# Performance work log

Hardware: AMD Instinct MI355X
Metric: run time of the kernel (lower is better)

The kernel has to match this reference:

```python
import jax, jax.numpy as jnp
import numpy as np

# ---- static config (matches init_kwargs) ----
B, N, DIM = 1, 2048, 1024
H, KVH, D = 16, 8, 64
GQ = H // KVH                 # grouped queries per kv head
WS = 64                       # sliding window size (causal, exact)
CBS, STRIDE = 32, 16          # compress block size / sliding stride
SEL_BLK, NSEL, NMEM = 32, 4, 1
NCB = N // STRIDE             # num compressed blocks (128)
NFB = N // SEL_BLK            # num fine blocks (64)
NCPF = SEL_BLK // STRIDE      # compressed blocks per fine block (2)
HID = CBS * D                 # compress MLP hidden (expand factor 1.0)
SCALE = D ** -0.5
THETA = 10000.0
NEG = -jnp.finfo(jnp.float32).max


def setup_inputs():
    key = jax.random.key(0)
    ks = jax.random.split(key, 16)
    s = 0.02
    r = lambda i, shape: jax.random.normal(ks[i], shape, jnp.float32) * s
    return {
        "inp": jax.random.normal(ks[0], (B, N, DIM), jnp.float32),
        "norm_g": jnp.ones((DIM,), jnp.float32),
        "Wqkv": r(1, (DIM, (H + 2 * KVH) * D)),
        "mem_kv": r(2, (2, KVH, NMEM, D)),
        "k_pos": r(3, (KVH, CBS, D)),
        "v_pos": r(4, (KVH, CBS, D)),
        "kW1": r(5, (CBS * D, HID)), "kb1": jnp.zeros((HID,), jnp.float32),
        "kW2": r(6, (HID, D)), "kb2": jnp.zeros((D,), jnp.float32),
        "vW1": r(7, (CBS * D, HID)), "vb1": jnp.zeros((HID,), jnp.float32),
        "vW2": r(8, (HID, D)), "vb2": jnp.zeros((D,), jnp.float32),
        "combW": r(9, (DIM, 3 * H)),
        "combB": jnp.tile(jnp.array([-2.0, -2.0, 2.0], jnp.float32), H),
        "Wout": r(10, (H * D, DIM)),
    }


def _rope(t):
    # lucidrains rotary-embedding-torch: interleaved adjacent-pair rotation
    inv_freq = 1.0 / (THETA ** (jnp.arange(0, D, 2, dtype=jnp.float32) / D))
    ang = jnp.arange(N, dtype=jnp.float32)[:, None] * inv_freq        # [N, D/2]
    cos = jnp.repeat(jnp.cos(ang), 2, axis=-1)                        # [N, D]
    sin = jnp.repeat(jnp.sin(ang), 2, axis=-1)
    t2 = t.reshape(*t.shape[:-1], D // 2, 2)
    rot = jnp.stack([-t2[..., 1], t2[..., 0]], axis=-1).reshape(t.shape)
    return t * cos + rot * sin


def _forward(inp, norm_g, Wqkv, mem_kv, k_pos, v_pos,
             kW1, kb1, kW2, kb2, vW1, vb1, vW2, vb2,
             combW, combB, Wout):
    # RMSNorm
    x = inp * jax.lax.rsqrt(jnp.mean(inp * inp, -1, keepdims=True)
                            + jnp.finfo(inp.dtype).eps) * norm_g
    qkv = x @ Wqkv
    q, k, v = jnp.split(qkv, [H * D, H * D + KVH * D], axis=-1)
    q = q.reshape(B, N, H, D).transpose(0, 2, 1, 3)      # b h n d
    k = k.reshape(B, N, KVH, D).transpose(0, 2, 1, 3)    # b kvh n d
    v = v.reshape(B, N, KVH, D).transpose(0, 2, 1, 3)

    # ---- compressed branch (overlapping windows, left zero pad) ----
    overlap = CBS - STRIDE
    kp = jnp.pad(k, ((0, 0), (0, 0), (overlap, 0), (0, 0)))
    vp = jnp.pad(v, ((0, 0), (0, 0), (overlap, 0), (0, 0)))
    widx = jnp.arange(NCB)[:, None] * STRIDE + jnp.arange(CBS)[None, :]  # [NCB, CBS]
    kw = kp[:, :, widx] + k_pos[None, :, None]   # b kvh w cbs d
    vw = vp[:, :, widx] + v_pos[None, :, None]

    def cmlp(t, W1, b1, W2, b2):
        t = t.reshape(B, KVH, NCB, CBS * D)
        return jax.nn.relu(t @ W1 + b1) @ W2 + b2       # b kvh w d

    ck = cmlp(kw, kW1, kb1, kW2, kb2)
    cv = cmlp(vw, vW1, vb1, vW2, vb2)
    ck = jnp.concatenate([jnp.broadcast_to(mem_kv[0], (B, KVH, NMEM, D)), ck], 2)
    cv = jnp.concatenate([jnp.broadcast_to(mem_kv[1], (B, KVH, NMEM, D)), cv], 2)

    qg = q.reshape(B, KVH, GQ, N, D)
    csim = jnp.einsum('bhgid,bhjd->bhgij', qg, ck) * SCALE   # no mask (cmask=None)
    cattn = jax.nn.softmax(csim, -1)
    cout = jnp.einsum('bhgij,bhjd->bhgid', cattn, cv).reshape(B, H, N, D)

    # rotary AFTER compressed attention (as in source)
    rq, rk = _rope(q), _rope(k)

    # ---- importance scores -> top-k fine block selection ----
    imp = csim[..., NMEM:].mean(2)                          # b kvh n NCB (share grouped q)
    imp = imp.reshape(B, KVH, N, NFB, NCPF).mean(-1)        # mean-pool to fine blocks
    q_blk = jnp.arange(N) // SEL_BLK
    diag = q_blk[:, None] == jnp.arange(NFB)[None, :]
    imp = jnp.where(diag[None, None], NEG, imp)             # mask own (diagonal) block
    imp = jax.nn.softmax(jnp.pad(imp, ((0, 0),) * 3 + ((1, 0),),
                                 constant_values=-1000.0), -1)[..., 1:]
    sel_val, sel_idx = jax.lax.top_k(imp, NSEL)             # b kvh n NSEL

    # ---- fine (block-selected) attention ----
    own = jnp.broadcast_to(q_blk[None, None, :, None], (B, KVH, N, 1))
    sel_idx = jnp.concatenate([sel_idx, own], -1)           # append own block
    fmask = jnp.repeat((sel_val > 1e-10)[..., None], SEL_BLK, -1)  # b kvh n NSEL blk
    causal_row = jnp.tril(jnp.ones((SEL_BLK, SEL_BLK), bool))[jnp.arange(N) % SEL_BLK]
    causal = jnp.broadcast_to(causal_row[None, None, :, None, :],
                              (B, KVH, N, 1, SEL_BLK))
    fmask = jnp.concatenate([fmask, causal], 3).reshape(B, KVH, N, (NSEL + 1) * SEL_BLK)

    fk_blocks = rk.reshape(B, KVH, NFB, SEL_BLK, D)
    fv_blocks = v.reshape(B, KVH, NFB, SEL_BLK, D)
    gather = jax.vmap(jax.vmap(lambda blocks, idx: blocks[idx]))  # over b, kvh
    fk = gather(fk_blocks, sel_idx).reshape(B, KVH, N, (NSEL + 1) * SEL_BLK, D)
    fv = gather(fv_blocks, sel_idx).reshape(B, KVH, N, (NSEL + 1) * SEL_BLK, D)

    rqg = rq.reshape(B, KVH, GQ, N, D)
    fsim = jnp.einsum('bhgid,bhijd->bhgij', rqg, fk) * SCALE
    fsim = jnp.where(fmask[:, :, None], fsim, NEG / 10)
    fattn = jax.nn.softmax(fsim, -1)
    fout = jnp.einsum('bhgij,bhijd->bhgid', fattn, fv).reshape(B, H, N, D)

    # ---- sliding window (causal, exact window size WS) ----
    NW = N // WS
    kp2 = jnp.pad(rk, ((0, 0), (0, 0), (WS, 0), (0, 0)))
    vp2 = jnp.pad(v, ((0, 0), (0, 0), (WS, 0), (0, 0)))
    kidx = jnp.arange(NW)[:, None] * WS + jnp.arange(2 * WS)[None, :]
    kwin = kp2[:, :, kidx]                                  # b kvh nw 2ws d
    vwin = vp2[:, :, kidx]
    qwin = rqg.reshape(B, KVH, GQ, NW, WS, D)
    ssim = jnp.einsum('bhgwid,bhwjd->bhgwij', qwin, kwin) * SCALE
    i = jnp.arange(WS)[:, None]
    j = jnp.arange(2 * WS)[None, :]
    diff = i - (j - WS)
    local_ok = (diff >= 0) & (diff < WS)                    # [WS, 2WS]
    keypos = jnp.arange(NW)[:, None, None] * WS + (jnp.arange(2 * WS) - WS)[None, None, :]
    smask = local_ok[None] & (keypos >= 0)                  # [NW, WS, 2WS]
    ssim = jnp.where(smask[None, None, None], ssim, NEG)
    sattn = jax.nn.softmax(ssim, -1)
    sout = jnp.einsum('bhgwij,bhwjd->bhgwid', sattn, vwin).reshape(B, H, N, D)

    # ---- learned strategy combination (compressed, fine, sliding) ----
    gates = jax.nn.sigmoid(x @ combW + combB).reshape(B, N, H, 3).transpose(0, 2, 1, 3)
    out = gates[..., 0:1] * cout + gates[..., 1:2] * fout + gates[..., 2:3] * sout
    out = out.transpose(0, 2, 1, 3).reshape(B, N, H * D) @ Wout
    return out


def reference(inp, norm_g, Wqkv, mem_kv, k_pos, v_pos,
              kW1, kb1, kW2, kb2, vW1, vb1, vW2, vb2,
              combW, combB, Wout):
    return _forward(inp, norm_g, Wqkv, mem_kv, k_pos, v_pos,
                    kW1, kb1, kW2, kb2, vW1, vb1, vW2, vb2,
                    combW, combB, Wout)
```

## Files before the change

### kernel.cpp

```cpp
#include <hip/hip_runtime.h>
#include <hip/hip_bf16.h>

#define NTOK 2048
#define DIM 1024
#define NH 16
#define KVH 8
#define GQ 2
#define HD 64
#define WS 64
#define CBS 32
#define STRIDE 16
#define SEL_BLK 32
#define NSEL 4
#define NMEM 1
#define NCB 128
#define NFB 64
#define HIDN 2048
#define SCALE 0.125f
#define NEGF (-3.4028234663852886e38f)
#define NEG10F (-3.4028234663852886e37f)

typedef __attribute__((ext_vector_type(8))) short bf16x8;
typedef __attribute__((ext_vector_type(4))) float f32x4;

__device__ __forceinline__ float bflo(unsigned u) { return __uint_as_float(u << 16); }
__device__ __forceinline__ float bfhi(unsigned u) { return __uint_as_float(u & 0xffff0000u); }
__device__ __forceinline__ void dot8(const float4& qa, const float4& qb, uint4 a, float& s) {
    s += qa.x * bflo(a.x) + qa.y * bfhi(a.x) + qa.z * bflo(a.y) + qa.w * bfhi(a.y) +
         qb.x * bflo(a.z) + qb.y * bfhi(a.z) + qb.z * bflo(a.w) + qb.w * bfhi(a.w);
}

__global__ __launch_bounds__(256) void rmsnorm_kernel(const float* __restrict__ inp,
                                                      const float* __restrict__ g,
                                                      float* __restrict__ x,
                                                      __hip_bfloat16* __restrict__ xb) {
    int n = blockIdx.x;
    const float* row = inp + (size_t)n * DIM;
    float ss = 0.f;
    for (int c = threadIdx.x; c < DIM; c += 256) { float v = row[c]; ss += v * v; }
    __shared__ float red[4];
    for (int o = 32; o; o >>= 1) ss += __shfl_down(ss, o, 64);
    if ((threadIdx.x & 63) == 0) red[threadIdx.x >> 6] = ss;
    __syncthreads();
    if (threadIdx.x == 0) red[0] = red[0] + red[1] + red[2] + red[3];
    __syncthreads();
    float rs = 1.0f / sqrtf(red[0] / (float)DIM + 1.1920928955078125e-07f);
    float* xr = x + (size_t)n * DIM;
    __hip_bfloat16* xbr = xb + (size_t)n * DIM;
    for (int c = threadIdx.x; c < DIM; c += 256) {
        float v = row[c] * rs * g[c];
        xr[c] = v;
        xbr[c] = __float2bfloat16(v);
    }
}

__device__ __forceinline__ void transpose_body(const float* __restrict__ B,
                                               __hip_bfloat16* __restrict__ Bt,
                                               int K, int N, int bx, int by) {
    __shared__ float tile[32][33];
    int n0 = bx * 32, k0 = by * 32;
    int x = threadIdx.x & 31, y = threadIdx.x >> 5;
    for (int i = 0; i < 4; i++) {
        int k = k0 + y + 8 * i, n = n0 + x;
        tile[y + 8 * i][x] = (k < K && n < N) ? B[(size_t)k * N + n] : 0.f;
    }
    __syncthreads();
    for (int i = 0; i < 4; i++) {
        int n = n0 + y + 8 * i, k = k0 + x;
        if (n < N && k < K) Bt[(size_t)n * K + k] = __float2bfloat16(tile[x][y + 8 * i]);
    }
}

__global__ __launch_bounds__(256) void transpose_all_kernel(
    const float* Wqkv, __hip_bfloat16* Wqkvt,
    const float* kW1, __hip_bfloat16* kW1t,
    const float* vW1, __hip_bfloat16* vW1t,
    const float* Wout, __hip_bfloat16* Woutt,
    const float* combW, __hip_bfloat16* combWt,
    const float* kW2, __hip_bfloat16* kW2t,
    const float* vW2, __hip_bfloat16* vW2t) {
    int b = blockIdx.x;
    if (b < 2048) { transpose_body(Wqkv, Wqkvt, 1024, 2048, b % 64, b / 64); return; }
    b -= 2048;
    if (b < 4096) { transpose_body(kW1, kW1t, 2048, 2048, b % 64, b / 64); return; }
    b -= 4096;
    if (b < 4096) { transpose_body(vW1, vW1t, 2048, 2048, b % 64, b / 64); return; }
    b -= 4096;
    if (b < 1024) { transpose_body(Wout, Woutt, 1024, 1024, b % 32, b / 32); return; }
    b -= 1024;
    if (b < 64) { transpose_body(combW, combWt, 1024, 48, b % 2, b / 2); return; }
    b -= 64;
    if (b < 128) { transpose_body(kW2, kW2t, 2048, 64, b % 2, b / 2); return; }
    b -= 128;
    transpose_body(vW2, vW2t, 2048, 64, b % 2, b / 2);
}

template <int ACT, int OUTBF16>
__device__ __forceinline__ void mfma_gemm_body(const __hip_bfloat16* __restrict__ A,
                                               const __hip_bfloat16* __restrict__ Bt,
                                               const float* __restrict__ bias,
                                               void* __restrict__ Cp,
                                               int M, int N, int K, int bx, int by) {
    __shared__ __align__(16) short As[128 * 32];
    __shared__ __align__(16) short Bs[128 * 32];
    int tid = threadIdx.x;
    int lane = tid & 63, wave = tid >> 6;
    int wm = (wave >> 1) * 64, wn = (wave & 1) * 64;
    int m0 = by * 128, n0 = bx * 128;
    f32x4 acc[4][4];
    for (int r = 0; r < 4; r++)
        for (int c = 0; c < 4; c++)
            acc[r][c] = (f32x4){0.f, 0.f, 0.f, 0.f};

    int r0 = tid >> 2, kc0 = tid & 3;
    int r1 = (tid + 256) >> 2, kc1 = tid & 3;

    for (int k0 = 0; k0 < K; k0 += 32) {
        __syncthreads();
        *(uint4*)&As[r0 * 32 + kc0 * 8] =
            *(const uint4*)(A + (size_t)(m0 + r0) * K + k0 + kc0 * 8);
        *(uint4*)&As[r1 * 32 + kc1 * 8] =
            *(const uint4*)(A + (size_t)(m0 + r1) * K + k0 + kc1 * 8);
        *(uint4*)&Bs[r0 * 32 + kc0 * 8] =
            *(const uint4*)(Bt + (size_t)(n0 + r0) * K + k0 + kc0 * 8);
        *(uint4*)&Bs[r1 * 32 + kc1 * 8] =
            *(const uint4*)(Bt + (size_t)(n0 + r1) * K + k0 + kc1 * 8);
        __syncthreads();
        bf16x8 af[4], bfr[4];
#pragma unroll
        for (int r = 0; r < 4; r++)
            af[r] = *(const bf16x8*)&As[(wm + r * 16 + (lane & 15)) * 32 + (lane >> 4) * 8];
#pragma unroll
        for (int c = 0; c < 4; c++)
            bfr[c] = *(const bf16x8*)&Bs[(wn + c * 16 + (lane & 15)) * 32 + (lane >> 4) * 8];
#pragma unroll
        for (int r = 0; r < 4; r++)
#pragma unroll
            for (int c = 0; c < 4; c++)
                acc[r][c] = __builtin_amdgcn_mfma_f32_16x16x32_bf16(af[r], bfr[c], acc[r][c], 0, 0, 0);
    }
    for (int r = 0; r < 4; r++) {
        int grow = m0 + wm + r * 16 + (lane >> 4) * 4;
        for (int c = 0; c < 4; c++) {
            int gcol = n0 + wn + c * 16 + (lane & 15);
            float bv = bias ? bias[gcol] : 0.f;
#pragma unroll
            for (int v = 0; v < 4; v++) {
                float val = acc[r][c][v] + bv;
                if (ACT == 1) val = fmaxf(val, 0.f);
                if (OUTBF16)
                    ((__hip_bfloat16*)Cp)[(size_t)(grow + v) * N + gcol] = __float2bfloat16(val);
                else
                    ((float*)Cp)[(size_t)(grow + v) * N + gcol] = val;
            }
        }
    }
}

template <int ACT, int OUTBF16>
__global__ __launch_bounds__(256) void mfma_gemm(const __hip_bfloat16* __restrict__ A,
                                                 const __hip_bfloat16* __restrict__ Bt,
                                                 const float* __restrict__ bias,
                                                 void* __restrict__ Cp,
                                                 int M, int N, int K) {
    mfma_gemm_body<ACT, OUTBF16>(A, Bt, bias, Cp, M, N, K, blockIdx.x, blockIdx.y);
}

__global__ __launch_bounds__(256) void mfma_gemm_pair(const __hip_bfloat16* A0,
                                                      const __hip_bfloat16* A1,
                                                      const __hip_bfloat16* Bt0,
                                                      const __hip_bfloat16* Bt1,
                                                      const float* bias0, const float* bias1,
                                                      __hip_bfloat16* C0, __hip_bfloat16* C1,
                                                      int M, int N, int K) {
    if (blockIdx.z == 0)
        mfma_gemm_body<1, 1>(A0, Bt0, bias0, C0, M, N, K, blockIdx.x, blockIdx.y);
    else
        mfma_gemm_body<1, 1>(A1, Bt1, bias1, C1, M, N, K, blockIdx.x, blockIdx.y);
}

__device__ __forceinline__ void skgemm_body(const __hip_bfloat16* __restrict__ A,
                                            const __hip_bfloat16* __restrict__ Bt,
                                            float* __restrict__ C,
                                            int M, int Nout, int K, int by, int bz, int nz) {
    __shared__ __align__(16) short As[128 * 32];
    __shared__ __align__(16) short Bs[64 * 32];
    int tid = threadIdx.x;
    int lane = tid & 63, wave = tid >> 6;
    int m0 = by * 128;
    int wm = wave * 32;
    int kchunk = K / nz;
    int kbase = bz * kchunk;
    f32x4 acc[2][4];
    for (int r = 0; r < 2; r++)
        for (int c = 0; c < 4; c++) acc[r][c] = (f32x4){0.f, 0.f, 0.f, 0.f};

    int ra = tid >> 2, kc = (tid & 3) * 8;
    for (int k0 = kbase; k0 < kbase + kchunk; k0 += 32) {
        __syncthreads();
        *(uint4*)&As[ra * 32 + kc] = *(const uint4*)(A + (size_t)(m0 + ra) * K + k0 + kc);
        *(uint4*)&As[(ra + 64) * 32 + kc] =
            *(const uint4*)(A + (size_t)(m0 + ra + 64) * K + k0 + kc);
        uint4 bv = (uint4){0u, 0u, 0u, 0u};
        if (ra < Nout) bv = *(const uint4*)(Bt + (size_t)ra * K + k0 + kc);
        *(uint4*)&Bs[ra * 32 + kc] = bv;
        __syncthreads();
        bf16x8 af[2], bfr[4];
#pragma unroll
        for (int r = 0; r < 2; r++)
            af[r] = *(const bf16x8*)&As[(wm + r * 16 + (lane & 15)) * 32 + (lane >> 4) * 8];
#pragma unroll
        for (int c = 0; c < 4; c++)
            bfr[c] = *(const bf16x8*)&Bs[(c * 16 + (lane & 15)) * 32 + (lane >> 4) * 8];
#pragma unroll
        for (int r = 0; r < 2; r++)
#pragma unroll
            for (int c = 0; c < 4; c++)
                acc[r][c] = __builtin_amdgcn_mfma_f32_16x16x32_bf16(af[r], bfr[c], acc[r][c], 0, 0, 0);
    }
    for (int r = 0; r < 2; r++) {
        int grow = m0 + wm + r * 16 + (lane >> 4) * 4;
        for (int c = 0; c < 4; c++) {
            int gcol = c * 16 + (lane & 15);
            if (gcol >= Nout) continue;
#pragma unroll
            for (int v = 0; v < 4; v++)
                atomicAdd(&C[(size_t)(grow + v) * Nout + gcol], acc[r][c][v]);
        }
    }
}

__global__ __launch_bounds__(256) void skgemm_kernel(const __hip_bfloat16* __restrict__ A,
                                                     const __hip_bfloat16* __restrict__ Bt,
                                                     float* __restrict__ C,
                                                     int M, int Nout, int K) {
    skgemm_body(A, Bt, C, M, Nout, K, blockIdx.y, blockIdx.z, gridDim.z);
}

__global__ __launch_bounds__(256) void skgemm_pair(const __hip_bfloat16* A0,
                                                   const __hip_bfloat16* A1,
                                                   const __hip_bfloat16* Bt0,
                                                   const __hip_bfloat16* Bt1,
                                                   float* C0, float* C1,
                                                   int M, int Nout, int K) {
    if (blockIdx.x == 0)
        skgemm_body(A0, Bt0, C0, M, Nout, K, blockIdx.y, blockIdx.z, gridDim.z);
    else
        skgemm_body(A1, Bt1, C1, M, Nout, K, blockIdx.y, blockIdx.z, gridDim.z);
}

__global__ __launch_bounds__(256) void initbias2_kernel(float* __restrict__ C0,
                                                        const float* __restrict__ b0,
                                                        float* __restrict__ C1,
                                                        const float* __restrict__ b1,
                                                        int M, int Nout) {
    int idx = blockIdx.x * 256 + threadIdx.x;
    int tot = M * Nout;
    if (idx < tot) C0[idx] = b0[idx % Nout];
    else if (idx < 2 * tot) { idx -= tot; C1[idx] = b1[idx % Nout]; }
}

__global__ __launch_bounds__(256) void initbias_kernel(float* __restrict__ C,
                                                       const float* __restrict__ bias,
                                                       int M, int Nout) {
    int idx = blockIdx.x * 256 + threadIdx.x;
    if (idx < M * Nout) C[idx] = bias[idx % Nout];
}

__global__ __launch_bounds__(256) void buildwin_kernel(const float* __restrict__ qkv,
                                                       const float* __restrict__ k_pos,
                                                       const float* __restrict__ v_pos,
                                                       __hip_bfloat16* __restrict__ kwflat,
                                                       __hip_bfloat16* __restrict__ vwflat) {
    size_t total = (size_t)(KVH * NCB) * HIDN;
    for (size_t e = (size_t)blockIdx.x * 256 + threadIdx.x; e < total;
         e += (size_t)gridDim.x * 256) {
        int r = (int)(e >> 11);
        int c = (int)(e & 2047);
        int j = c >> 6, d = c & 63;
        int h = r >> 7, i = r & 127;
        int p = i * STRIDE + j - (CBS - STRIDE);
        float kb = k_pos[((size_t)h * CBS + j) * HD + d];
        float vb = v_pos[((size_t)h * CBS + j) * HD + d];
        float kv = 0.f, vv = 0.f;
        if (p >= 0) {
            kv = qkv[(size_t)p * 2048 + 1024 + h * HD + d];
            vv = qkv[(size_t)p * 2048 + 1536 + h * HD + d];
        }
        kwflat[e] = __float2bfloat16(kv + kb);
        vwflat[e] = __float2bfloat16(vv + vb);
    }
}

__global__ __launch_bounds__(256) void rope_kernel(const float* __restrict__ qkv,
                                                   float* __restrict__ rq,
                                                   __hip_bfloat16* __restrict__ rk,
                                                   __hip_bfloat16* __restrict__ vt) {
    int n = blockIdx.x;
    int t = threadIdx.x;
    for (int idx = t; idx < NH * 32; idx += 256) {
        int h = idx >> 5, f = idx & 31;
        float inv = exp2f((float)f * -0.41524101186092f);
        float ang = (float)n * inv;
        float cc = cosf(ang), ssn = sinf(ang);
        float a = qkv[(size_t)n * 2048 + h * HD + 2 * f];
        float b = qkv[(size_t)n * 2048 + h * HD + 2 * f + 1];
        float* o = rq + ((size_t)h * NTOK + n) * HD + 2 * f;
        o[0] = a * cc - b * ssn;
        o[1] = b * cc + a * ssn;
    }
    for (int idx = t; idx < KVH * 32; idx += 256) {
        int h = idx >> 5, f = idx & 31;
        float inv = exp2f((float)f * -0.41524101186092f);
        float ang = (float)n * inv;
        float cc = cosf(ang), ssn = sinf(ang);
        float a = qkv[(size_t)n * 2048 + 1024 + h * HD + 2 * f];
        float b = qkv[(size_t)n * 2048 + 1024 + h * HD + 2 * f + 1];
        __hip_bfloat16* o = rk + ((size_t)h * NTOK + n) * HD + 2 * f;
        o[0] = __float2bfloat16(a * cc - b * ssn);
        o[1] = __float2bfloat16(b * cc + a * ssn);
    }
    for (int idx = t; idx < KVH * HD; idx += 256) {
        int h = idx >> 6, d = idx & 63;
        vt[((size_t)h * NTOK + n) * HD + d] =
            __float2bfloat16(qkv[(size_t)n * 2048 + 1536 + h * HD + d]);
    }
}

__global__ __launch_bounds__(256) void cattn2_kernel(const float* __restrict__ qkv,
                                                     const float* __restrict__ ckraw,
                                                     const float* __restrict__ cvraw,
                                                     const float* __restrict__ memkv,
                                                     float* __restrict__ cout,
                                                     float* __restrict__ imp) {
    int h = blockIdx.x >> 6;
    int i0 = (blockIdx.x & 63) * 32;
    int t = threadIdx.x;
    __shared__ float qs[64][68];
    __shared__ float sc[64][132];
    __shared__ float scratch[32 * 68];
    __shared__ float memk[64], memv[64];
    __shared__ float impm[32], impd[32];

    for (int idx = t; idx < 4096; idx += 256) {
        int row = idx >> 6, d = idx & 63;
        int g = row >> 5, qi = row & 31;
        qs[row][d] = qkv[(size_t)(i0 + qi) * 2048 + (h * 2 + g) * 64 + d];
    }
    if (t < 64) { memk[t] = memkv[h * 64 + t]; memv[t] = memkv[(8 + h) * 64 + t]; }
    __syncthreads();
    if (t < 64) {
        float s = 0.f;
        for (int d = 0; d < 64; d++) s += qs[t][d] * memk[d];
        sc[t][0] = s * SCALE;
    }
    int rg = t >> 3, kg = t & 7;
    for (int c = 0; c < 4; c++) {
        __syncthreads();
        for (int idx = t; idx < 2048; idx += 256) {
            int jj = idx >> 6, d = idx & 63;
            scratch[jj * 68 + d] = ckraw[((size_t)h * 128 + c * 32 + jj) * 64 + d];
        }
        __syncthreads();
        float a0[4] = {}, a1[4] = {};
        for (int d = 0; d < 64; d += 4) {
            float4 q0 = *(const float4*)&qs[rg * 2][d];
            float4 q1 = *(const float4*)&qs[rg * 2 + 1][d];
#pragma unroll
            for (int kk = 0; kk < 4; kk++) {
                float4 kv = *(const float4*)&scratch[(kg + kk * 8) * 68 + d];
                a0[kk] += q0.x * kv.x + q0.y * kv.y + q0.z * kv.z + q0.w * kv.w;
                a1[kk] += q1.x * kv.x + q1.y * kv.y + q1.z * kv.z + q1.w * kv.w;
            }
        }
#pragma unroll
        for (int kk = 0; kk < 4; kk++) {
            sc[rg * 2][1 + c * 32 + kg + kk * 8] = a0[kk] * SCALE;
            sc[rg * 2 + 1][1 + c * 32 + kg + kk * 8] = a1[kk] * SCALE;
        }
    }
    __syncthreads();
    for (int idx = t; idx < 2048; idx += 256) {
        int qi = idx >> 6, fb = idx & 63;
        float v = 0.25f * (sc[qi][1 + 2 * fb] + sc[qi][2 + 2 * fb] +
                           sc[32 + qi][1 + 2 * fb] + sc[32 + qi][2 + 2 * fb]);
        if (fb == ((i0 + qi) >> 5)) v = NEGF;
        scratch[qi * 66 + fb] = v;
    }
    __syncthreads();
    if (t < 32) {
        float m = -1000.f;
        for (int j = 0; j < 64; j++) m = fmaxf(m, scratch[t * 66 + j]);
        float den = expf(-1000.f - m);
        for (int j = 0; j < 64; j++) den += expf(scratch[t * 66 + j] - m);
        impm[t] = m; impd[t] = 1.f / den;
    } else if (t >= 64 && t < 128) {
        int r = t - 64;
        float m = NEGF;
        for (int j = 0; j < 129; j++) m = fmaxf(m, sc[r][j]);
        float den = 0.f;
        for (int j = 0; j < 129; j++) { float e = expf(sc[r][j] - m); sc[r][j] = e; den += e; }
        float inv = 1.f / den;
        for (int j = 0; j < 129; j++) sc[r][j] *= inv;
    }
    __syncthreads();
    for (int idx = t; idx < 2048; idx += 256) {
        int qi = idx >> 6, fb = idx & 63;
        imp[((size_t)h * NTOK + i0 + qi) * 64 + fb] =
            expf(scratch[qi * 66 + fb] - impm[qi]) * impd[qi];
    }
    int dg = t & 7;
    float o0[8], o1[8];
    {
        float p0 = sc[rg * 2][0], p1 = sc[rg * 2 + 1][0];
#pragma unroll
        for (int dd = 0; dd < 8; dd++) {
            float v = memv[dg + dd * 8];
            o0[dd] = p0 * v;
            o1[dd] = p1 * v;
        }
    }
    for (int c = 0; c < 4; c++) {
        __syncthreads();
        for (int idx = t; idx < 2048; idx += 256) {
            int jj = idx >> 6, d = idx & 63;
            scratch[jj * 68 + d] = cvraw[((size_t)h * 128 + c * 32 + jj) * 64 + d];
        }
        __syncthreads();
        for (int jj = 0; jj < 32; jj++) {
            float p0 = sc[rg * 2][1 + c * 32 + jj];
            float p1 = sc[rg * 2 + 1][1 + c * 32 + jj];
#pragma unroll
            for (int dd = 0; dd < 8; dd++) {
                float v = scratch[jj * 68 + dg + dd * 8];
                o0[dd] += p0 * v;
                o1[dd] += p1 * v;
            }
        }
    }
    {
        int row = rg * 2;
        int g = row >> 5, qi = row & 31;
        int g2 = (row + 1) >> 5, qi2 = (row + 1) & 31;
#pragma unroll
        for (int dd = 0; dd < 8; dd++) {
            cout[(((size_t)(h * 2 + g)) * NTOK + i0 + qi) * 64 + dd * 8 + dg] = o0[dd];
            cout[(((size_t)(h * 2 + g2)) * NTOK + i0 + qi2) * 64 + dd * 8 + dg] = o1[dd];
        }
    }
}

__global__ __launch_bounds__(256) void topk_kernel(const float* __restrict__ imp,
                                                   int* __restrict__ selidx,
                                                   int* __restrict__ selmask) {
    int idx = blockIdx.x * 256 + threadIdx.x;
    if (idx >= KVH * NTOK) return;
    const float* ip = imp + (size_t)idx * NFB;
    float v[NFB];
    for (int j = 0; j < NFB; j++) v[j] = ip[j];
    unsigned long long taken = 0ull;
    int mk = 0;
    int i = idx & 2047;
    for (int p = 0; p < NSEL; p++) {
        float bv = NEGF;
        int bi = 0;
        for (int j = 0; j < NFB; j++) {
            if (!((taken >> j) & 1ull) && v[j] > bv) { bv = v[j]; bi = j; }
        }
        taken |= 1ull << bi;
        selidx[(size_t)idx * 5 + p] = bi;
        if (bv > 1e-10f) mk |= 1 << p;
    }
    selidx[(size_t)idx * 5 + 4] = i >> 5;
    selmask[idx] = mk;
}

__global__ __launch_bounds__(256) void attn_fused_kernel(const float* __restrict__ rq,
                                                         const __hip_bfloat16* __restrict__ rk,
                                                         const __hip_bfloat16* __restrict__ vt,
                                                         const int* __restrict__ selidx,
                                                         const int* __restrict__ selmask,
                                                         float* __restrict__ fout,
                                                         float* __restrict__ sout) {
    int ws = threadIdx.x >> 6, lane = threadIdx.x & 63;
    __shared__ float sp[4][2][160];
    __shared__ int sel[4][5];
    __shared__ int smk[4];
    float* p0 = sp[ws][0];
    float* p1 = sp[ws][1];

    int kq = lane >> 2, c = lane & 3;
    int kv8 = lane >> 3, c8 = lane & 7;

    if (blockIdx.x < 4096) {
        int wid = blockIdx.x * 4 + ws;
        int h = wid >> 11, i = wid & 2047;
        if (lane < 5) sel[ws][lane] = selidx[((size_t)h * NTOK + i) * 5 + lane];
        if (lane == 5) smk[ws] = selmask[h * NTOK + i];

        const float* q0p = rq + ((size_t)(h * 2 + 0) * NTOK + i) * 64 + c * 16;
        const float* q1p = rq + ((size_t)(h * 2 + 1) * NTOK + i) * 64 + c * 16;
        float4 q0[4], q1[4];
#pragma unroll
        for (int u = 0; u < 4; u++) {
            q0[u] = *(const float4*)(q0p + u * 4);
            q1[u] = *(const float4*)(q1p + u * 4);
        }
        __syncthreads();
        int mk = smk[ws];
        int iq = i & 31;
#pragma unroll
        for (int kt = 0; kt < 10; kt++) {
            int slot = kt >> 1;
            int blk = sel[ws][slot];
            int key = kt * 16 + kq;
            int jj = key & 31;
            int kpos = blk * 32 + jj;
            bool valid = (slot < 4) ? (((mk >> slot) & 1) != 0) : (jj <= iq);
            const __hip_bfloat16* kr = rk + ((size_t)h * NTOK + kpos) * 64 + c * 16;
            float s0 = 0.f, s1 = 0.f;
            uint4 a = *(const uint4*)(kr);
            uint4 b = *(const uint4*)(kr + 8);
            dot8(q0[0], q0[1], a, s0); dot8(q0[2], q0[3], b, s0);
            dot8(q1[0], q1[1], a, s1); dot8(q1[2], q1[3], b, s1);
            s0 += __shfl_xor(s0, 1); s0 += __shfl_xor(s0, 2);
            s1 += __shfl_xor(s1, 1); s1 += __shfl_xor(s1, 2);
            if (c == 0) {
                p0[key] = valid ? s0 * SCALE : NEG10F;
                p1[key] = valid ? s1 * SCALE : NEG10F;
            }
        }
        __syncthreads();
        {
            float a0 = p0[lane], b0 = p0[lane + 64];
            float c0 = (lane < 32) ? p0[lane + 128] : NEG10F;
            float a1 = p1[lane], b1 = p1[lane + 64];
            float c1 = (lane < 32) ? p1[lane + 128] : NEG10F;
            float m0 = fmaxf(fmaxf(a0, b0), c0);
            float m1 = fmaxf(fmaxf(a1, b1), c1);
#pragma unroll
            for (int o = 1; o < 64; o <<= 1) {
                m0 = fmaxf(m0, __shfl_xor(m0, o));
                m1 = fmaxf(m1, __shfl_xor(m1, o));
            }
            float ea0 = __expf(a0 - m0), eb0 = __expf(b0 - m0), ec0 = (lane < 32) ? __expf(c0 - m0) : 0.f;
            float ea1 = __expf(a1 - m1), eb1 = __expf(b1 - m1), ec1 = (lane < 32) ? __expf(c1 - m1) : 0.f;
            float d0 = ea0 + eb0 + ec0;
            float d1 = ea1 + eb1 + ec1;
#pragma unroll
            for (int o = 1; o < 64; o <<= 1) {
                d0 += __shfl_xor(d0, o);
                d1 += __shfl_xor(d1, o);
            }
            float inv0 = 1.f / d0, inv1 = 1.f / d1;
            p0[lane] = ea0 * inv0; p0[lane + 64] = eb0 * inv0;
            p1[lane] = ea1 * inv1; p1[lane + 64] = eb1 * inv1;
            if (lane < 32) { p0[lane + 128] = ec0 * inv0; p1[lane + 128] = ec1 * inv1; }
        }
        __syncthreads();
        float o0[8] = {}, o1[8] = {};
#pragma unroll
        for (int slot = 0; slot < 5; slot++) {
            const __hip_bfloat16* vbase = vt + ((size_t)h * NTOK + sel[ws][slot] * 32) * 64;
#pragma unroll
            for (int pass = 0; pass < 4; pass++) {
                int j = pass * 8 + kv8;
                uint4 v = *(const uint4*)(vbase + j * 64 + c8 * 8);
                float pa = p0[slot * 32 + j], pb = p1[slot * 32 + j];
                float e0 = bflo(v.x), e1 = bfhi(v.x), e2 = bflo(v.y), e3 = bfhi(v.y);
                float e4 = bflo(v.z), e5 = bfhi(v.z), e6 = bflo(v.w), e7 = bfhi(v.w);
                o0[0] = fmaf(pa, e0, o0[0]); o0[1] = fmaf(pa, e1, o0[1]);
                o0[2] = fmaf(pa, e2, o0[2]); o0[3] = fmaf(pa, e3, o0[3]);
                o0[4] = fmaf(pa, e4, o0[4]); o0[5] = fmaf(pa, e5, o0[5]);
                o0[6] = fmaf(pa, e6, o0[6]); o0[7] = fmaf(pa, e7, o0[7]);
                o1[0] = fmaf(pb, e0, o1[0]); o1[1] = fmaf(pb, e1, o1[1]);
                o1[2] = fmaf(pb, e2, o1[2]); o1[3] = fmaf(pb, e3, o1[3]);
                o1[4] = fmaf(pb, e4, o1[4]); o1[5] = fmaf(pb, e5, o1[5]);
                o1[6] = fmaf(pb, e6, o1[6]); o1[7] = fmaf(pb, e7, o1[7]);
            }
        }
#pragma unroll
        for (int o = 8; o <= 32; o <<= 1)
#pragma unroll
            for (int d = 0; d < 8; d++) {
                o0[d] += __shfl_xor(o0[d], o);
                o1[d] += __shfl_xor(o1[d], o);
            }
        if (kv8 == 0) {
            float* f0 = fout + ((size_t)(h * 2 + 0) * NTOK + i) * 64 + c8 * 8;
            float* f1 = fout + ((size_t)(h * 2 + 1) * NTOK + i) * 64 + c8 * 8;
            *(float4*)(f0) = (float4){o0[0], o0[1], o0[2], o0[3]};
            *(float4*)(f0 + 4) = (float4){o0[4], o0[5], o0[6], o0[7]};
            *(float4*)(f1) = (float4){o1[0], o1[1], o1[2], o1[3]};
            *(float4*)(f1 + 4) = (float4){o1[4], o1[5], o1[6], o1[7]};
        }
    } else {
        int wid = (blockIdx.x - 4096) * 4 + ws;
        int h = wid >> 11, i = wid & 2047;
        const float* q0p = rq + ((size_t)(h * 2 + 0) * NTOK + i) * 64 + c * 16;
        const float* q1p = rq + ((size_t)(h * 2 + 1) * NTOK + i) * 64 + c * 16;
        float4 q0[4], q1[4];
#pragma unroll
        for (int u = 0; u < 4; u++) {
            q0[u] = *(const float4*)(q0p + u * 4);
            q1[u] = *(const float4*)(q1p + u * 4);
        }
#pragma unroll
        for (int kt = 0; kt < 4; kt++) {
            int key = kt * 16 + kq;
            int kpos = i - 63 + key;
            int kp = kpos < 0 ? 0 : kpos;
            const __hip_bfloat16* kr = rk + ((size_t)h * NTOK + kp) * 64 + c * 16;
            float s0 = 0.f, s1 = 0.f;
            uint4 a = *(const uint4*)(kr);
            uint4 b = *(const uint4*)(kr + 8);
            dot8(q0[0], q0[1], a, s0); dot8(q0[2], q0[3], b, s0);
            dot8(q1[0], q1[1], a, s1); dot8(q1[2], q1[3], b, s1);
            s0 += __shfl_xor(s0, 1); s0 += __shfl_xor(s0, 2);
            s1 += __shfl_xor(s1, 1); s1 += __shfl_xor(s1, 2);
            if (c == 0) {
                p0[key] = (kpos >= 0) ? s0 * SCALE : NEG10F;
                p1[key] = (kpos >= 0) ? s1 * SCALE : NEG10F;
            }
        }
        __syncthreads();
        {
            float a0 = p0[lane], a1 = p1[lane];
            float m0 = a0, m1 = a1;
#pragma unroll
            for (int o = 1; o < 64; o <<= 1) {
                m0 = fmaxf(m0, __shfl_xor(m0, o));
                m1 = fmaxf(m1, __shfl_xor(m1, o));
            }
            float e0 = __expf(a0 - m0), e1 = __expf(a1 - m1);
            float d0 = e0, d1 = e1;
#pragma unroll
            for (int o = 1; o < 64; o <<= 1) {
                d0 += __shfl_xor(d0, o);
                d1 += __shfl_xor(d1, o);
            }
            p0[lane] = e0 / d0;
            p1[lane] = e1 / d1;
        }
        __syncthreads();
        int base = i - 63;
        float o0[8] = {}, o1[8] = {};
        const __hip_bfloat16* vbase = vt + (size_t)h * NTOK * 64;
#pragma unroll
        for (int pass = 0; pass < 8; pass++) {
            int j = pass * 8 + kv8;
            int kpos = base + j;
            int kp = kpos < 0 ? 0 : kpos;
            uint4 v = *(const uint4*)(vbase + (size_t)kp * 64 + c8 * 8);
            float pa = p0[j], pb = p1[j];
            float e0 = bflo(v.x), e1 = bfhi(v.x), e2 = bflo(v.y), e3 = bfhi(v.y);
            float e4 = bflo(v.z), e5 = bfhi(v.z), e6 = bflo(v.w), e7 = bfhi(v.w);
            o0[0] = fmaf(pa, e0, o0[0]); o0[1] = fmaf(pa, e1, o0[1]);
            o0[2] = fmaf(pa, e2, o0[2]); o0[3] = fmaf(pa, e3, o0[3]);
            o0[4] = fmaf(pa, e4, o0[4]); o0[5] = fmaf(pa, e5, o0[5]);
            o0[6] = fmaf(pa, e6, o0[6]); o0[7] = fmaf(pa, e7, o0[7]);
            o1[0] = fmaf(pb, e0, o1[0]); o1[1] = fmaf(pb, e1, o1[1]);
            o1[2] = fmaf(pb, e2, o1[2]); o1[3] = fmaf(pb, e3, o1[3]);
            o1[4] = fmaf(pb, e4, o1[4]); o1[5] = fmaf(pb, e5, o1[5]);
            o1[6] = fmaf(pb, e6, o1[6]); o1[7] = fmaf(pb, e7, o1[7]);
        }
#pragma unroll
        for (int o = 8; o <= 32; o <<= 1)
#pragma unroll
            for (int d = 0; d < 8; d++) {
                o0[d] += __shfl_xor(o0[d], o);
                o1[d] += __shfl_xor(o1[d], o);
            }
        if (kv8 == 0) {
            float* s0p = sout + ((size_t)(h * 2 + 0) * NTOK + i) * 64 + c8 * 8;
            float* s1p = sout + ((size_t)(h * 2 + 1) * NTOK + i) * 64 + c8 * 8;
            *(float4*)(s0p) = (float4){o0[0], o0[1], o0[2], o0[3]};
            *(float4*)(s0p + 4) = (float4){o0[4], o0[5], o0[6], o0[7]};
            *(float4*)(s1p) = (float4){o1[0], o1[1], o1[2], o1[3]};
            *(float4*)(s1p + 4) = (float4){o1[4], o1[5], o1[6], o1[7]};
        }
    }
}

__global__ __launch_bounds__(256) void combine_kernel(const float* __restrict__ gateslin,
                                                      const float* __restrict__ cout,
                                                      const float* __restrict__ fout,
                                                      const float* __restrict__ sout,
                                                      __hip_bfloat16* __restrict__ att) {
    int n = blockIdx.x;
    for (int c = threadIdx.x; c < NH * HD; c += 256) {
        int hd = c >> 6, d = c & 63;
        float g0 = 1.f / (1.f + expf(-gateslin[(size_t)n * (NH * 3) + hd * 3 + 0]));
        float g1 = 1.f / (1.f + expf(-gateslin[(size_t)n * (NH * 3) + hd * 3 + 1]));
        float g2 = 1.f / (1.f + expf(-gateslin[(size_t)n * (NH * 3) + hd * 3 + 2]));
        size_t o = ((size_t)hd * NTOK + n) * HD + d;
        att[(size_t)n * (NH * HD) + c] =
            __float2bfloat16(g0 * cout[o] + g1 * fout[o] + g2 * sout[o]);
    }
}

extern "C" void kernel_launch(void* const* d_in, const int* in_sizes, int n_in,
                              void* d_out, int out_size, void* d_ws, size_t ws_size,
                              hipStream_t stream) {
    const float* inp    = (const float*)d_in[0];
    const float* norm_g = (const float*)d_in[1];
    const float* Wqkv   = (const float*)d_in[2];
    const float* mem_kv = (const float*)d_in[3];
    const float* k_pos  = (const float*)d_in[4];
    const float* v_pos  = (const float*)d_in[5];
    const float* kW1    = (const float*)d_in[6];
    const float* kb1    = (const float*)d_in[7];
    const float* kW2    = (const float*)d_in[8];
    const float* kb2    = (const float*)d_in[9];
    const float* vW1    = (const float*)d_in[10];
    const float* vb1    = (const float*)d_in[11];
    const float* vW2    = (const float*)d_in[12];
    const float* vb2    = (const float*)d_in[13];
    const float* combW  = (const float*)d_in[14];
    const float* combB  = (const float*)d_in[15];
    const float* Wout   = (const float*)d_in[16];
    float* out = (float*)d_out;

    char* base = (char*)d_ws;
    size_t off = 0;
    auto alloc = [&](size_t bytes) {
        void* p = base + off;
        off += (bytes + 255) & ~(size_t)255;
        return p;
    };
    float* x            = (float*)alloc((size_t)NTOK * DIM * 4);
    __hip_bfloat16* xb  = (__hip_bfloat16*)alloc((size_t)NTOK * DIM * 2);
    float* qkv          = (float*)alloc((size_t)NTOK * 2048 * 4);
    __hip_bfloat16* Wqkvt = (__hip_bfloat16*)alloc((size_t)2048 * 1024 * 2);
    __hip_bfloat16* kW1t  = (__hip_bfloat16*)alloc((size_t)2048 * 2048 * 2);
    __hip_bfloat16* vW1t  = (__hip_bfloat16*)alloc((size_t)2048 * 2048 * 2);
    __hip_bfloat16* Woutt = (__hip_bfloat16*)alloc((size_t)1024 * 1024 * 2);
    __hip_bfloat16* combWt = (__hip_bfloat16*)alloc((size_t)48 * 1024 * 2);
    __hip_bfloat16* kW2t  = (__hip_bfloat16*)alloc((size_t)64 * 2048 * 2);
    __hip_bfloat16* vW2t  = (__hip_bfloat16*)alloc((size_t)64 * 2048 * 2);
    __hip_bfloat16* kwflat = (__hip_bfloat16*)alloc((size_t)KVH * NCB * HIDN * 2);
    __hip_bfloat16* vwflat = (__hip_bfloat16*)alloc((size_t)KVH * NCB * HIDN * 2);
    __hip_bfloat16* hidkb = (__hip_bfloat16*)alloc((size_t)KVH * NCB * HIDN * 2);
    __hip_bfloat16* hidvb = (__hip_bfloat16*)alloc((size_t)KVH * NCB * HIDN * 2);
    float* ckraw        = (float*)alloc((size_t)KVH * NCB * HD * 4);
    float* cvraw        = (float*)alloc((size_t)KVH * NCB * HD * 4);
    float* rq           = (float*)alloc((size_t)NH * NTOK * HD * 4);
    __hip_bfloat16* rk  = (__hip_bfloat16*)alloc((size_t)KVH * NTOK * HD * 2);
    __hip_bfloat16* vt  = (__hip_bfloat16*)alloc((size_t)KVH * NTOK * HD * 2);
    float* coutb        = (float*)alloc((size_t)NH * NTOK * HD * 4);
    float* foutb        = (float*)alloc((size_t)NH * NTOK * HD * 4);
    float* soutb        = (float*)alloc((size_t)NH * NTOK * HD * 4);
    float* impb         = (float*)alloc((size_t)KVH * NTOK * NFB * 4);
    float* gatesb       = (float*)alloc((size_t)NTOK * NH * 3 * 4);
    __hip_bfloat16* attb = (__hip_bfloat16*)alloc((size_t)NTOK * DIM * 2);
    int* selidx         = (int*)alloc((size_t)KVH * NTOK * 5 * 4);
    int* selmask        = (int*)alloc((size_t)KVH * NTOK * 4);
    (void)ws_size; (void)in_sizes; (void)n_in; (void)out_size;

    rmsnorm_kernel<<<NTOK, 256, 0, stream>>>(inp, norm_g, x, xb);
    transpose_all_kernel<<<11584, 256, 0, stream>>>(Wqkv, Wqkvt, kW1, kW1t, vW1, vW1t,
                                                    Wout, Woutt, combW, combWt,
                                                    kW2, kW2t, vW2, vW2t);
    mfma_gemm<0, 0><<<dim3(16, 16), 256, 0, stream>>>(xb, Wqkvt, nullptr, qkv, 2048, 2048, 1024);
    initbias_kernel<<<(NTOK * 48 + 255) / 256, 256, 0, stream>>>(gatesb, combB, NTOK, 48);
    skgemm_kernel<<<dim3(1, 16, 4), 256, 0, stream>>>(xb, combWt, gatesb, 2048, 48, 1024);
    buildwin_kernel<<<4096, 256, 0, stream>>>(qkv, k_pos, v_pos, kwflat, vwflat);
    mfma_gemm_pair<<<dim3(16, 8, 2), 256, 0, stream>>>(kwflat, vwflat, kW1t, vW1t,
                                                       kb1, vb1, hidkb, hidvb,
                                                       1024, 2048, 2048);
    initbias2_kernel<<<(2 * 1024 * 64 + 255) / 256, 256, 0, stream>>>(ckraw, kb2, cvraw, vb2, 1024, 64);
    skgemm_pair<<<dim3(2, 8, 8), 256, 0, stream>>>(hidkb, hidvb, kW2t, vW2t,
                                                   ckraw, cvraw, 1024, 64, 2048);
    rope_kernel<<<NTOK, 256, 0, stream>>>(qkv, rq, rk, vt);
    cattn2_kernel<<<KVH * (NTOK / 32), 256, 0, stream>>>(qkv, ckraw, cvraw, mem_kv, coutb, impb);
    topk_kernel<<<(KVH * NTOK) / 256, 256, 0, stream>>>(impb, selidx, selmask);
    attn_fused_kernel<<<8192, 256, 0, stream>>>(rq, rk, vt, selidx, selmask, foutb, soutb);
    combine_kernel<<<NTOK, 256, 0, stream>>>(gatesb, coutb, foutb, soutb, attb);
    mfma_gemm<0, 0><<<dim3(8, 16), 256, 0, stream>>>(attb, Woutt, nullptr, out, 2048, 1024, 1024);
}
```

Before: 423.8 us.

## Fuse top-k selection into compressed attention and use direct global-to-LDS loads

Top-k block selection moves into the compressed-attention kernel and runs on the raw scores, so the importance matrix is never written to global memory and one kernel launch goes away. Selection compares raw scores, which gives the same order as softmax probabilities, and the mask threshold is recomputed from the softmax. The GEMM kernels now stage tiles with global_load_lds instead of loading into registers and then storing to LDS. Fast __expf replaces expf. The top-k loop runs serially on 32 threads per block, which adds latency to that kernel.

```diff
diff --git a/kernel.cpp b/kernel.cpp
--- a/kernel.cpp
+++ b/kernel.cpp
@@ -28,6 +28,11 @@
 __device__ __forceinline__ void dot8(const float4& qa, const float4& qb, uint4 a, float& s) {
     s += qa.x * bflo(a.x) + qa.y * bfhi(a.x) + qa.z * bflo(a.y) + qa.w * bfhi(a.y) +
          qb.x * bflo(a.z) + qb.y * bfhi(a.z) + qb.z * bflo(a.w) + qb.w * bfhi(a.w);
+}
+
+__device__ __forceinline__ void gload_lds16(const void* g, void* l) {
+    __builtin_amdgcn_global_load_lds((const __attribute__((address_space(1))) unsigned*)g,
+                                     (__attribute__((address_space(3))) unsigned*)l, 16, 0, 0);
 }
 
 __global__ __launch_bounds__(256) void rmsnorm_kernel(const float* __restrict__ inp,
@@ -112,19 +117,15 @@
         for (int c = 0; c < 4; c++)
             acc[r][c] = (f32x4){0.f, 0.f, 0.f, 0.f};
 
-    int r0 = tid >> 2, kc0 = tid & 3;
-    int r1 = (tid + 256) >> 2, kc1 = tid & 3;
+    int r0 = tid >> 2, kc0 = (tid & 3) * 8;
+    int r1 = r0 + 64;
 
     for (int k0 = 0; k0 < K; k0 += 32) {
         __syncthreads();
-        *(uint4*)&As[r0 * 32 + kc0 * 8] =
-            *(const uint4*)(A + (size_t)(m0 + r0) * K + k0 + kc0 * 8);
-        *(uint4*)&As[r1 * 32 + kc1 * 8] =
-            *(const uint4*)(A + (size_t)(m0 + r1) * K + k0 + kc1 * 8);
-        *(uint4*)&Bs[r0 * 32 + kc0 * 8] =
-            *(const uint4*)(Bt + (size_t)(n0 + r0) * K + k0 + kc0 * 8);
-        *(uint4*)&Bs[r1 * 32 + kc1 * 8] =
-            *(const uint4*)(Bt + (size_t)(n0 + r1) * K + k0 + kc1 * 8);
+        gload_lds16(A + (size_t)(m0 + r0) * K + k0 + kc0, &As[r0 * 32 + kc0]);
+        gload_lds16(A + (size_t)(m0 + r1) * K + k0 + kc0, &As[r1 * 32 + kc0]);
+        gload_lds16(Bt + (size_t)(n0 + r0) * K + k0 + kc0, &Bs[r0 * 32 + kc0]);
+        gload_lds16(Bt + (size_t)(n0 + r1) * K + k0 + kc0, &Bs[r1 * 32 + kc0]);
         __syncthreads();
         bf16x8 af[4], bfr[4];
 #pragma unroll
@@ -196,14 +197,12 @@
         for (int c = 0; c < 4; c++) acc[r][c] = (f32x4){0.f, 0.f, 0.f, 0.f};
 
     int ra = tid >> 2, kc = (tid & 3) * 8;
+    int rb = ra < Nout ? ra : Nout - 1;
     for (int k0 = kbase; k0 < kbase + kchunk; k0 += 32) {
         __syncthreads();
-        *(uint4*)&As[ra * 32 + kc] = *(const uint4*)(A + (size_t)(m0 + ra) * K + k0 + kc);
-        *(uint4*)&As[(ra + 64) * 32 + kc] =
-            *(const uint4*)(A + (size_t)(m0 + ra + 64) * K + k0 + kc);
-        uint4 bv = (uint4){0u, 0u, 0u, 0u};
-        if (ra < Nout) bv = *(const uint4*)(Bt + (size_t)ra * K + k0 + kc);
-        *(uint4*)&Bs[ra * 32 + kc] = bv;
+        gload_lds16(A + (size_t)(m0 + ra) * K + k0 + kc, &As[ra * 32 + kc]);
+        gload_lds16(A + (size_t)(m0 + ra + 64) * K + k0 + kc, &As[(ra + 64) * 32 + kc]);
+        gload_lds16(Bt + (size_t)rb * K + k0 + kc, &Bs[ra * 32 + kc]);
         __syncthreads();
         bf16x8 af[2], bfr[4];
 #pragma unroll
@@ -332,7 +331,8 @@
                                                      const float* __restrict__ cvraw,
                                                      const float* __restrict__ memkv,
                                                      float* __restrict__ cout,
-                                                     float* __restrict__ imp) {
+                                                     int* __restrict__ selidx,
+                                                     int* __restrict__ selmask) {
     int h = blockIdx.x >> 6;
     int i0 = (blockIdx.x & 63) * 32;
     int t = threadIdx.x;
@@ -340,7 +340,6 @@
     __shared__ float sc[64][132];
     __shared__ float scratch[32 * 68];
     __shared__ float memk[64], memv[64];
-    __shared__ float impm[32], impd[32];
 
     for (int idx = t; idx < 4096; idx += 256) {
         int row = idx >> 6, d = idx & 63;
@@ -389,26 +388,37 @@
     }
     __syncthreads();
     if (t < 32) {
+        float* row = &scratch[t * 66];
         float m = -1000.f;
-        for (int j = 0; j < 64; j++) m = fmaxf(m, scratch[t * 66 + j]);
-        float den = expf(-1000.f - m);
-        for (int j = 0; j < 64; j++) den += expf(scratch[t * 66 + j] - m);
-        impm[t] = m; impd[t] = 1.f / den;
+        for (int j = 0; j < 64; j++) m = fmaxf(m, row[j]);
+        float den = __expf(-1000.f - m);
+        for (int j = 0; j < 64; j++) den += __expf(row[j] - m);
+        float invd = 1.f / den;
+        unsigned long long taken = 0ull;
+        int mk = 0;
+        size_t base = ((size_t)h * NTOK + i0 + t) * 5;
+        for (int p = 0; p < NSEL; p++) {
+            float bv = NEGF;
+            int bi = 0;
+            for (int j = 0; j < 64; j++) {
+                if (!((taken >> j) & 1ull) && row[j] > bv) { bv = row[j]; bi = j; }
+            }
+            taken |= 1ull << bi;
+            selidx[base + p] = bi;
+            if (__expf(bv - m) * invd > 1e-10f) mk |= 1 << p;
+        }
+        selidx[base + 4] = (i0 + t) >> 5;
+        selmask[h * NTOK + i0 + t] = mk;
     } else if (t >= 64 && t < 128) {
         int r = t - 64;
         float m = NEGF;
         for (int j = 0; j < 129; j++) m = fmaxf(m, sc[r][j]);
         float den = 0.f;
-        for (int j = 0; j < 129; j++) { float e = expf(sc[r][j] - m); sc[r][j] = e; den += e; }
+        for (int j = 0; j < 129; j++) { float e = __expf(sc[r][j] - m); sc[r][j] = e; den += e; }
         float inv = 1.f / den;
         for (int j = 0; j < 129; j++) sc[r][j] *= inv;
     }
     __syncthreads();
-    for (int idx = t; idx < 2048; idx += 256) {
-        int qi = idx >> 6, fb = idx & 63;
-        imp[((size_t)h * NTOK + i0 + qi) * 64 + fb] =
-            expf(scratch[qi * 66 + fb] - impm[qi]) * impd[qi];
-    }
     int dg = t & 7;
     float o0[8], o1[8];
     {
@@ -448,31 +458,6 @@
             cout[(((size_t)(h * 2 + g2)) * NTOK + i0 + qi2) * 64 + dd * 8 + dg] = o1[dd];
         }
     }
-}
-
-__global__ __launch_bounds__(256) void topk_kernel(const float* __restrict__ imp,
-                                                   int* __restrict__ selidx,
-                                                   int* __restrict__ selmask) {
-    int idx = blockIdx.x * 256 + threadIdx.x;
-    if (idx >= KVH * NTOK) return;
-    const float* ip = imp + (size_t)idx * NFB;
-    float v[NFB];
-    for (int j = 0; j < NFB; j++) v[j] = ip[j];
-    unsigned long long taken = 0ull;
-    int mk = 0;
-    int i = idx & 2047;
-    for (int p = 0; p < NSEL; p++) {
-        float bv = NEGF;
-        int bi = 0;
-        for (int j = 0; j < NFB; j++) {
-            if (!((taken >> j) & 1ull) && v[j] > bv) { bv = v[j]; bi = j; }
-        }
-        taken |= 1ull << bi;
-        selidx[(size_t)idx * 5 + p] = bi;
-        if (bv > 1e-10f) mk |= 1 << p;
-    }
-    selidx[(size_t)idx * 5 + 4] = i >> 5;
-    selmask[idx] = mk;
 }
 
 __global__ __launch_bounds__(256) void attn_fused_kernel(const float* __restrict__ rq,
@@ -750,7 +735,6 @@
     float* coutb        = (float*)alloc((size_t)NH * NTOK * HD * 4);
     float* foutb        = (float*)alloc((size_t)NH * NTOK * HD * 4);
     float* soutb        = (float*)alloc((size_t)NH * NTOK * HD * 4);
-    float* impb         = (float*)alloc((size_t)KVH * NTOK * NFB * 4);
     float* gatesb       = (float*)alloc((size_t)NTOK * NH * 3 * 4);
     __hip_bfloat16* attb = (__hip_bfloat16*)alloc((size_t)NTOK * DIM * 2);
     int* selidx         = (int*)alloc((size_t)KVH * NTOK * 5 * 4);
@@ -772,8 +756,8 @@
     skgemm_pair<<<dim3(2, 8, 8), 256, 0, stream>>>(hidkb, hidvb, kW2t, vW2t,
                                                    ckraw, cvraw, 1024, 64, 2048);
     rope_kernel<<<NTOK, 256, 0, stream>>>(qkv, rq, rk, vt);
-    cattn2_kernel<<<KVH * (NTOK / 32), 256, 0, stream>>>(qkv, ckraw, cvraw, mem_kv, coutb, impb);
-    topk_kernel<<<(KVH * NTOK) / 256, 256, 0, stream>>>(impb, selidx, selmask);
+    cattn2_kernel<<<KVH * (NTOK / 32), 256, 0, stream>>>(qkv, ckraw, cvraw, mem_kv,
+                                                         coutb, selidx, selmask);
     attn_fused_kernel<<<8192, 256, 0, stream>>>(rq, rk, vt, selidx, selmask, foutb, soutb);
     combine_kernel<<<NTOK, 256, 0, stream>>>(gatesb, coutb, foutb, soutb, attb);
     mfma_gemm<0, 0><<<dim3(8, 16), 256, 0, stream>>>(attb, Woutt, nullptr, out, 2048, 1024, 1024);
```

Result: faster. 411.8 us (-2.8%).
